# Performance work log

Measured on AMD Instinct MI355X. Metric: run time of the kernel, lower is better.

## Reference

```python
import jax, jax.numpy as jnp
import numpy as np

N_READ = 200000
N_INTRON = 50000
N_EDGES = 2000000
DIMS = [(10, 64), (64, 128), (128, 128), (128, 128), (128, 128), (128, 128)]


def setup_inputs() -> dict:
    key = jax.random.key(0)
    ks = jax.random.split(key, 4 + 2 * len(DIMS) + 3)
    inp = {}
    inp['h_read'] = jax.random.normal(ks[0], (N_READ, 10), dtype=jnp.float32)
    inp['edge_src'] = jax.random.randint(ks[1], (N_EDGES,), 0, N_READ, dtype=jnp.int32)
    inp['edge_dst'] = jax.random.randint(ks[2], (N_EDGES,), 0, N_INTRON, dtype=jnp.int32)
    for i, (fin, fout) in enumerate(DIMS):
        # Glorot-uniform like DGL GraphConv init
        lim = np.sqrt(6.0 / (fin + fout)).astype(np.float32)
        inp[f'W{i}'] = jax.random.uniform(ks[3 + 2 * i], (fin, fout), jnp.float32, -lim, lim)
        inp[f'b{i}'] = jnp.zeros((fout,), jnp.float32)
    inp['atts'] = jax.random.normal(ks[-3], (6,), dtype=jnp.float32)
    inp['fc_w'] = jax.random.normal(ks[-2], (128, 2), dtype=jnp.float32) * 0.05
    inp['fc_b'] = jnp.zeros((2,), jnp.float32)
    return inp


def _graph_conv(feat_src, W, b, src, dst, n_src, n_dst):
    # DGL GraphConv with norm='both': D_src^{-1/2} then sum-aggregate then D_dst^{-1/2}, then linear.
    ones = jnp.ones((src.shape[0],), feat_src.dtype)
    out_deg = jnp.maximum(jax.ops.segment_sum(ones, src, num_segments=n_src), 1.0)
    in_deg = jnp.maximum(jax.ops.segment_sum(ones, dst, num_segments=n_dst), 1.0)
    h = feat_src * jax.lax.rsqrt(out_deg)[:, None]          # [n_src, d]
    agg = jax.ops.segment_sum(h[src], dst, num_segments=n_dst)  # gather + scatter-add
    agg = agg * jax.lax.rsqrt(in_deg)[:, None]
    return agg @ W + b


def reference(h_read, edge_src, edge_dst, W0, W1, W2, W3, W4, W5,
              b0, b1, b2, b3, b4, b5, atts, fc_w, fc_b):
    Ws = [W0, W1, W2, W3, W4, W5]
    bs = [b0, b1, b2, b3, b4, b5]
    h_r = h_read
    h_i = None
    for i in range(6):
        gate = jax.nn.sigmoid(atts[i])
        if i % 2 == 0:
            # read -> intron
            h_i = _graph_conv(h_r, Ws[i], bs[i], edge_src, edge_dst, N_READ, N_INTRON)
            h_i = jax.nn.relu(h_i * gate)
        else:
            # intron -> read (reversed edges)
            h_r = _graph_conv(h_i, Ws[i], bs[i], edge_dst, edge_src, N_INTRON, N_READ)
            h_r = jax.nn.relu(h_r * gate)
    return h_r @ fc_w + fc_b  # [N_READ, 2]
```

## Files before the change

### kernel.cpp

```cpp
#include <hip/hip_runtime.h>

#define N_READ   200000
#define N_INTRON 50000
#define N_EDGES  2000000

#define NB    256
#define EPB   ((N_EDGES + NB - 1) / NB)
#define NBUK  782
#define SH_I  6
#define SH_R  8
#define NITEMS (NBUK * NB)
#define CSH   13
#define NGRP  (N_READ / 4)

typedef float f4 __attribute__((ext_vector_type(4)));
typedef float f2 __attribute__((ext_vector_type(2)));
typedef unsigned u32x4 __attribute__((ext_vector_type(4)));
typedef unsigned short u16x4 __attribute__((ext_vector_type(4)));

static __device__ __forceinline__ unsigned short f2bf(float x) {
  unsigned u = __builtin_bit_cast(unsigned, x);
  u = (u + 0x7fffu + ((u >> 16) & 1u)) >> 16;
  return (unsigned short)u;
}
static __device__ __forceinline__ float blo(unsigned u) {
  return __builtin_bit_cast(float, u << 16);
}
static __device__ __forceinline__ float bhi(unsigned u) {
  return __builtin_bit_cast(float, u & 0xffff0000u);
}

__global__ void kb_hist(const int* __restrict__ src, const int* __restrict__ dst,
                        int* __restrict__ histI, int* __restrict__ histR) {
  __shared__ int hI[1024], hR[1024];
  const int t = threadIdx.x, b = blockIdx.x;
  for (int k = t; k < 1024; k += 256) { hI[k] = 0; hR[k] = 0; }
  __syncthreads();
  const int s0 = b * EPB;
  const int s1 = (s0 + EPB < N_EDGES) ? s0 + EPB : N_EDGES;
  for (int i = s0 + t; i < s1; i += 256) {
    atomicAdd(&hI[dst[i] >> SH_I], 1);
    atomicAdd(&hR[src[i] >> SH_R], 1);
  }
  __syncthreads();
  for (int k = t; k < NBUK; k += 256) {
    histI[k * NB + b] = hI[k];
    histR[k * NB + b] = hR[k];
  }
}

__global__ void k_scan1(const int* __restrict__ cnt, int* __restrict__ rp,
                        int* __restrict__ bsum, int n) {
  __shared__ int lds[256];
  int t = threadIdx.x;
  int i = blockIdx.x * 256 + t;
  int v = (i < n) ? cnt[i] : 0;
  lds[t] = v;
  __syncthreads();
  for (int off = 1; off < 256; off <<= 1) {
    int x = (t >= off) ? lds[t - off] : 0;
    __syncthreads();
    lds[t] += x;
    __syncthreads();
  }
  if (i < n) rp[i + 1] = lds[t];
  if (t == 255) bsum[blockIdx.x] = lds[255];
}

__global__ void k_scan2(int* __restrict__ bsum, int nb) {
  __shared__ int lds[1024];
  int t = threadIdx.x;
  int v = (t < nb) ? bsum[t] : 0;
  lds[t] = v;
  __syncthreads();
  for (int off = 1; off < 1024; off <<= 1) {
    int x = (t >= off) ? lds[t - off] : 0;
    __syncthreads();
    lds[t] += x;
    __syncthreads();
  }
  if (t < nb) bsum[t] = lds[t];
}

__global__ void k_scan3b(int* __restrict__ rp, const int* __restrict__ bsum, int n) {
  int i = blockIdx.x * 256 + threadIdx.x;
  if (i >= n) return;
  int off = (blockIdx.x == 0) ? 0 : bsum[blockIdx.x - 1];
  rp[i + 1] += off;
  if (i == 0) rp[0] = 0;
}

__global__ void kb_scatter(const int* __restrict__ src, const int* __restrict__ dst,
                           const int* __restrict__ scanI, const int* __restrict__ scanR,
                           unsigned* __restrict__ bI, unsigned* __restrict__ bR) {
  __shared__ int cI[1024], cR[1024];
  const int t = threadIdx.x, b = blockIdx.x;
  for (int k = t; k < NBUK; k += 256) {
    cI[k] = scanI[k * NB + b];
    cR[k] = scanR[k * NB + b];
  }
  __syncthreads();
  const int s0 = b * EPB;
  const int s1 = (s0 + EPB < N_EDGES) ? s0 + EPB : N_EDGES;
  for (int i = s0 + t; i < s1; i += 256) {
    int s = src[i], d = dst[i];
    int slot = atomicAdd(&cI[d >> SH_I], 1);
    bI[slot] = ((unsigned)s << SH_I) | (unsigned)(d & 63);
    int slot2 = atomicAdd(&cR[s >> SH_R], 1);
    bR[slot2] = ((unsigned)d << SH_R) | (unsigned)(s & 255);
  }
}

template <int NBINS, int SH, typename PT>
__global__ void kb_fine(const unsigned* __restrict__ bk, const int* __restrict__ scan,
                        int* __restrict__ rp, float* __restrict__ rs,
                        PT* __restrict__ csr, int n_nodes) {
  __shared__ int hist[NBINS], cur[NBINS], lds[256];
  const int t = threadIdx.x, k = blockIdx.x;
  for (int j = t; j < NBINS; j += 256) hist[j] = 0;
  __syncthreads();
  const int s0 = scan[k * NB];
  const int e0 = (k + 1 < NBUK) ? scan[(k + 1) * NB] : N_EDGES;
  for (int i = s0 + t; i < e0; i += 256) atomicAdd(&hist[bk[i] & (NBINS - 1)], 1);
  __syncthreads();
  int v = (t < NBINS) ? hist[t] : 0;
  lds[t] = v;
  __syncthreads();
  for (int off = 1; off < 256; off <<= 1) {
    int x = (t >= off) ? lds[t - off] : 0;
    __syncthreads();
    lds[t] += x;
    __syncthreads();
  }
  if (t < NBINS) {
    int base = s0 + lds[t] - hist[t];
    cur[t] = base;
    int n = k * NBINS + t;
    if (n < n_nodes) {
      rp[n] = base;
      rs[n] = rsqrtf((float)(hist[t] > 0 ? hist[t] : 1));
    }
  }
  if (k == NBUK - 1 && t == 0) rp[n_nodes] = N_EDGES;
  __syncthreads();
  for (int i = s0 + t; i < e0; i += 256) {
    unsigned v2 = bk[i];
    int slot = atomicAdd(&cur[v2 & (NBINS - 1)], 1);
    csr[slot] = (PT)(v2 >> SH);
  }
}

__global__ void kb_fine_r(const unsigned* __restrict__ bk, const int* __restrict__ scan,
                          int* __restrict__ rpg, float* __restrict__ rs,
                          unsigned* __restrict__ recs, int n_nodes) {
  __shared__ int cnt2[64 * 8], cur2[64 * 8], lds[256], cntn[256];
  const int t = threadIdx.x, k = blockIdx.x;
  for (int j = t; j < 512; j += 256) cnt2[j] = 0;
  cntn[t] = 0;
  __syncthreads();
  const int s0 = scan[k * NB];
  const int e0 = (k + 1 < NBUK) ? scan[(k + 1) * NB] : N_EDGES;
  for (int i = s0 + t; i < e0; i += 256) {
    unsigned v = bk[i];
    int rl = v & 255;
    int c = (int)(v >> 8) >> CSH;
    atomicAdd(&cnt2[(rl >> 2) * 8 + c], 1);
    atomicAdd(&cntn[rl], 1);
  }
  __syncthreads();
  int tg = 0;
  if (t < 64) {
#pragma unroll
    for (int c = 0; c < 8; ++c) tg += cnt2[t * 8 + c];
  }
  lds[t] = tg;
  __syncthreads();
  for (int off = 1; off < 64; off <<= 1) {
    int x = (t >= off) ? lds[t - off] : 0;
    __syncthreads();
    lds[t] += x;
    __syncthreads();
  }
  if (t < 64) {
    int base = s0 + lds[t] - tg;
    int run = base;
#pragma unroll
    for (int c = 0; c < 8; ++c) { cur2[t * 8 + c] = run; run += cnt2[t * 8 + c]; }
    int g = k * 64 + t;
    if (g < NGRP) rpg[g] = base;
  }
  {
    int n = k * 256 + t;
    if (n < n_nodes) {
      int d = cntn[t];
      rs[n] = rsqrtf((float)(d > 0 ? d : 1));
    }
  }
  if (k == NBUK - 1 && t == 0) rpg[NGRP] = N_EDGES;
  __syncthreads();
  for (int i = s0 + t; i < e0; i += 256) {
    unsigned v = bk[i];
    int rl = v & 255;
    unsigned intron = v >> 8;
    int c = (int)intron >> CSH;
    int slot = atomicAdd(&cur2[(rl >> 2) * 8 + c], 1);
    recs[slot] = ((unsigned)(rl & 3) << 16) | intron;
  }
}

__global__ void k_prep_h0(const float* __restrict__ h_read, const float* __restrict__ rs_r,
                          float* __restrict__ h16) {
  int i = blockIdx.x * blockDim.x + threadIdx.x;
  if (i >= N_READ * 16) return;
  int n = i >> 4, c = i & 15;
  h16[i] = (c < 10) ? h_read[n * 10 + c] * rs_r[n] : 0.0f;
}

__global__ void k_prep_W0(const float* __restrict__ W0, float* __restrict__ W0p) {
  int i = blockIdx.x * blockDim.x + threadIdx.x;
  if (i >= 16 * 64) return;
  int k = i >> 6, j = i & 63;
  W0p[i] = (k < 10) ? W0[k * 64 + j] : 0.0f;
}

template <int DIN>
__launch_bounds__(256)
__global__ void kx_transform(const unsigned* __restrict__ h32,
                             const float* __restrict__ W,
                             unsigned short* __restrict__ g,
                             int n_src) {
  constexpr int RS = DIN + 4;
  constexpr int HC = DIN / 2;
  __shared__ float rows[32 * RS];
  const int tid = threadIdx.x;
  const int nbase = blockIdx.x * 32;
  for (int idx = tid; idx < 32 * HC; idx += 256) {
    int r = idx / HC, cp = idx % HC;
    int n = nbase + r;
    unsigned u = (n < n_src) ? h32[(size_t)n * HC + cp] : 0u;
    rows[r * RS + cp * 2] = blo(u);
    rows[r * RS + cp * 2 + 1] = bhi(u);
  }
  __syncthreads();
  const int jg = tid % 32, ng = tid / 32;
  const int j0 = jg * 4;
  f4 acc[4];
#pragma unroll
  for (int p = 0; p < 4; ++p) acc[p] = (f4){0.f, 0.f, 0.f, 0.f};
#pragma unroll 2
  for (int k = 0; k < DIN; k += 4) {
    f4 w[4];
#pragma unroll
    for (int u = 0; u < 4; ++u) w[u] = *(const f4*)&W[(k + u) * 128 + j0];
#pragma unroll
    for (int p = 0; p < 4; ++p) {
      f4 r = *(const f4*)&rows[(ng + p * 8) * RS + k];
#pragma unroll
      for (int u = 0; u < 4; ++u) acc[p] += r[u] * w[u];
    }
  }
#pragma unroll
  for (int p = 0; p < 4; ++p) {
    const int n = nbase + ng + p * 8;
    if (n < n_src) {
      u16x4 o = {f2bf(acc[p][0]), f2bf(acc[p][1]), f2bf(acc[p][2]), f2bf(acc[p][3])};
      *(u16x4*)&g[(size_t)n * 128 + j0] = o;
    }
  }
}

template <bool FC>
__launch_bounds__(256)
__global__ void k_sweep2(const unsigned* __restrict__ g32,
                         const int* __restrict__ rpg,
                         const unsigned* __restrict__ recs,
                         const float* __restrict__ rs_dst,
                         const float* __restrict__ bias,
                         const float* __restrict__ atts, int li,
                         unsigned* __restrict__ hout32,
                         const float* __restrict__ fcw, const float* __restrict__ fcb,
                         float* __restrict__ fcout) {
  const int tid = threadIdx.x;
  const int wave = tid >> 6, lane = tid & 63;
  const int slot = lane >> 4, lc = lane & 15;
  const int group = blockIdx.x * 4 + wave;
  const int s = rpg[group], e = rpg[group + 1];

  f4 aA[4], aB[4];
#pragma unroll
  for (int n = 0; n < 4; ++n) {
    aA[n] = (f4){0.f, 0.f, 0.f, 0.f};
    aB[n] = (f4){0.f, 0.f, 0.f, 0.f};
  }

  for (int base = s; base < e; base += 64) {
    int idx = base + lane;
    if (idx > N_EDGES - 1) idx = N_EDGES - 1;
    unsigned rec = recs[idx];
    int m = e - base;
    if (m > 64) m = 64;
    for (int r = 0; r < m; r += 4) {
      unsigned rc = (unsigned)__shfl((int)rec, r + slot, 64);
      int id = (int)(rc & 0xffffu);
      int nl = (int)((rc >> 16) & 3u);
      float act = ((r + slot) < m) ? 1.f : 0.f;
      u32x4 v = *(const u32x4*)(g32 + (size_t)id * 64 + lc * 4);
      f4 vA = {blo(v.x), bhi(v.x), blo(v.y), bhi(v.y)};
      f4 vB = {blo(v.z), bhi(v.z), blo(v.w), bhi(v.w)};
      float m0 = (nl == 0) ? act : 0.f;
      float m1 = (nl == 1) ? act : 0.f;
      float m2 = (nl == 2) ? act : 0.f;
      float m3 = (nl == 3) ? act : 0.f;
      aA[0] += vA * m0; aB[0] += vB * m0;
      aA[1] += vA * m1; aB[1] += vB * m1;
      aA[2] += vA * m2; aB[2] += vB * m2;
      aA[3] += vA * m3; aB[3] += vB * m3;
    }
  }

#pragma unroll
  for (int n = 0; n < 4; ++n) {
#pragma unroll
    for (int j = 0; j < 4; ++j) {
      aA[n][j] += __shfl_xor(aA[n][j], 16);
      aA[n][j] += __shfl_xor(aA[n][j], 32);
      aB[n][j] += __shfl_xor(aB[n][j], 16);
      aB[n][j] += __shfl_xor(aB[n][j], 32);
    }
  }

  f4 sA = aA[0], sB = aB[0];
  if (slot == 1) { sA = aA[1]; sB = aB[1]; }
  if (slot == 2) { sA = aA[2]; sB = aB[2]; }
  if (slot == 3) { sA = aA[3]; sB = aB[3]; }
  const int n = group * 4 + slot;
  const float rsd = rs_dst[n];
  const float gate = 1.f / (1.f + __expf(-atts[li]));
  f4 bA = *(const f4*)&bias[lc * 8];
  f4 bB = *(const f4*)&bias[lc * 8 + 4];
  f4 vA = (sA * rsd + bA) * gate;
  f4 vB = (sB * rsd + bB) * gate;
#pragma unroll
  for (int j = 0; j < 4; ++j) {
    vA[j] = fmaxf(vA[j], 0.f);
    vB[j] = fmaxf(vB[j], 0.f);
  }
  if constexpr (!FC) {
    vA *= rsd;
    vB *= rsd;
    u32x4 o;
    o.x = (unsigned)f2bf(vA[0]) | ((unsigned)f2bf(vA[1]) << 16);
    o.y = (unsigned)f2bf(vA[2]) | ((unsigned)f2bf(vA[3]) << 16);
    o.z = (unsigned)f2bf(vB[0]) | ((unsigned)f2bf(vB[1]) << 16);
    o.w = (unsigned)f2bf(vB[2]) | ((unsigned)f2bf(vB[3]) << 16);
    *(u32x4*)(hout32 + (size_t)n * 64 + lc * 4) = o;
  } else {
    f4 w0 = *(const f4*)&fcw[lc * 16];
    f4 w1 = *(const f4*)&fcw[lc * 16 + 4];
    f4 w2 = *(const f4*)&fcw[lc * 16 + 8];
    f4 w3 = *(const f4*)&fcw[lc * 16 + 12];
    float s0 = vA[0] * w0[0] + vA[1] * w0[2] + vA[2] * w1[0] + vA[3] * w1[2]
             + vB[0] * w2[0] + vB[1] * w2[2] + vB[2] * w3[0] + vB[3] * w3[2];
    float s1 = vA[0] * w0[1] + vA[1] * w0[3] + vA[2] * w1[1] + vA[3] * w1[3]
             + vB[0] * w2[1] + vB[1] * w2[3] + vB[2] * w3[1] + vB[3] * w3[3];
    s0 += __shfl_xor(s0, 1); s0 += __shfl_xor(s0, 2);
    s0 += __shfl_xor(s0, 4); s0 += __shfl_xor(s0, 8);
    s1 += __shfl_xor(s1, 1); s1 += __shfl_xor(s1, 2);
    s1 += __shfl_xor(s1, 4); s1 += __shfl_xor(s1, 8);
    if (lc == 0) {
      fcout[n * 2] = s0 + fcb[0];
      fcout[n * 2 + 1] = s1 + fcb[1];
    }
  }
}

template <int DIN, int DOUT, bool BF16SRC, typename ET>
__launch_bounds__(256)
__global__ void k_layer(const void* __restrict__ hsrc_, const int* __restrict__ rp,
                        const ET* __restrict__ eidx, const float* __restrict__ rs_dst,
                        const float* __restrict__ W, const float* __restrict__ bias,
                        const float* __restrict__ atts, int li,
                        const float* __restrict__ rs_next,
                        void* __restrict__ hout_, int n_dst) {
  constexpr int NT = 32;
  constexpr int RSTR = DIN + 4;
  __shared__ float rows[NT * RSTR];
  __shared__ int rpl[NT + 1];
  const int tid = threadIdx.x;
  const int nbase = blockIdx.x * NT;
  const int team = tid >> 6, lane = tid & 63;
  const float* hs_f = (const float*)hsrc_;
  const unsigned short* hs_b = (const unsigned short*)hsrc_;

  constexpr int LPS = (DIN * (BF16SRC ? 2 : 4)) / 16;
  constexpr int SLOTS = 64 / LPS;
  const int slot = lane / LPS, lc = lane % LPS;

  if (tid <= NT) {
    int nn = nbase + tid;
    if (nn > n_dst) nn = n_dst;
    rpl[tid] = rp[nn];
  }
  __syncthreads();

  {
    int p0 = rpl[team * 8] + lane;
    if (p0 > N_EDGES - 1) p0 = N_EDGES - 1;
    int idsC = (int)eidx[p0];

    for (int t8 = 0; t8 < 8; ++t8) {
      const int t = team * 8 + t8;
      const int e0 = rpl[t], e1 = rpl[t + 1];
      const int deg = e1 - e0;
      int pn = e1 + lane;
      if (pn > N_EDGES - 1) pn = N_EDGES - 1;
      int idsN = (int)eidx[pn];

      f4 accA = {0.f, 0.f, 0.f, 0.f};
      f4 accB = {0.f, 0.f, 0.f, 0.f};
      int processed = 0;
      while (processed < deg) {
        int m = deg - processed;
        if (m > 64) m = 64;
        if (processed > 0) {
          int pr = e0 + processed + lane;
          if (pr > N_EDGES - 1) pr = N_EDGES - 1;
          idsC = (int)eidx[pr];
        }
        for (int r = 0; r < m; r += SLOTS) {
          int idv = __shfl(idsC, r + slot, 64);
          if constexpr (BF16SRC) {
            u32x4 v = *(const u32x4*)(hs_b + (size_t)idv * DIN + lc * 8);
            if (r + slot < m) {
              accA[0] += blo(v.x); accA[1] += bhi(v.x);
              accA[2] += blo(v.y); accA[3] += bhi(v.y);
              accB[0] += blo(v.z); accB[1] += bhi(v.z);
              accB[2] += blo(v.w); accB[3] += bhi(v.w);
            }
          } else {
            f4 v = *(const f4*)(hs_f + (size_t)idv * DIN + lc * 4);
            if (r + slot < m) accA += v;
          }
        }
        processed += m;
      }
      idsC = idsN;

#pragma unroll
      for (int off = LPS; off < 64; off <<= 1) {
#pragma unroll
        for (int k = 0; k < 4; ++k) accA[k] += __shfl_xor(accA[k], off);
        if constexpr (BF16SRC) {
#pragma unroll
          for (int k = 0; k < 4; ++k) accB[k] += __shfl_xor(accB[k], off);
        }
      }
      if (slot == 0) {
        const int n = nbase + t;
        const float rsd = (n < n_dst) ? rs_dst[n] : 0.f;
        if constexpr (BF16SRC) {
          *(f4*)&rows[t * RSTR + lc * 8] = accA * rsd;
          *(f4*)&rows[t * RSTR + lc * 8 + 4] = accB * rsd;
        } else {
          *(f4*)&rows[t * RSTR + lc * 4] = accA * rsd;
        }
      }
    }
  }
  __syncthreads();

  constexpr int JG = DOUT / 4;
  constexpr int NG = 256 / JG;
  constexpr int NPT = NT / NG;
  const int jg = tid % JG, ng = tid / JG;
  const int j0 = jg * 4;

  f4 acc[NPT];
#pragma unroll
  for (int p = 0; p < NPT; ++p) acc[p] = (f4){0.f, 0.f, 0.f, 0.f};

#pragma unroll 2
  for (int k = 0; k < DIN; k += 4) {
    f4 w[4];
#pragma unroll
    for (int u = 0; u < 4; ++u) w[u] = *(const f4*)&W[(k + u) * DOUT + j0];
#pragma unroll
    for (int p = 0; p < NPT; ++p) {
      f4 r = *(const f4*)&rows[(ng + p * NG) * RSTR + k];
#pragma unroll
      for (int u = 0; u < 4; ++u) acc[p] += r[u] * w[u];
    }
  }

  const float gate = 1.f / (1.f + __expf(-atts[li]));
  const f4 b4 = *(const f4*)&bias[j0];
#pragma unroll
  for (int p = 0; p < NPT; ++p) {
    const int nl = ng + p * NG;
    const int n = nbase + nl;
    if (n < n_dst) {
      f4 v = (acc[p] + b4) * gate;
#pragma unroll
      for (int c = 0; c < 4; ++c) v[c] = fmaxf(v[c], 0.f);
      if (rs_next) v *= rs_next[n];
      u16x4 o = {f2bf(v[0]), f2bf(v[1]), f2bf(v[2]), f2bf(v[3])};
      *(u16x4*)&((unsigned short*)hout_)[(size_t)n * DOUT + j0] = o;
    }
  }
}

extern "C" void kernel_launch(void* const* d_in, const int* in_sizes, int n_in,
                              void* d_out, int out_size, void* d_ws, size_t ws_size,
                              hipStream_t stream) {
  const float* h_read = (const float*)d_in[0];
  const int* esrc = (const int*)d_in[1];
  const int* edst = (const int*)d_in[2];
  const float* W0 = (const float*)d_in[3];
  const float* b0 = (const float*)d_in[4];
  const float* W1 = (const float*)d_in[5];
  const float* b1 = (const float*)d_in[6];
  const float* W2 = (const float*)d_in[7];
  const float* b2 = (const float*)d_in[8];
  const float* W3 = (const float*)d_in[9];
  const float* b3 = (const float*)d_in[10];
  const float* W4 = (const float*)d_in[11];
  const float* b4 = (const float*)d_in[12];
  const float* W5 = (const float*)d_in[13];
  const float* b5 = (const float*)d_in[14];
  const float* atts = (const float*)d_in[15];
  const float* fcw = (const float*)d_in[16];
  const float* fcb = (const float*)d_in[17];
  float* out = (float*)d_out;

  char* w = (char*)d_ws;
  size_t off = 0;
  auto alloc = [&](size_t bytes) -> void* {
    void* p = w + off;
    off += (bytes + 15) & ~(size_t)15;
    return p;
  };
  int* rp_i = (int*)alloc((N_INTRON + 1) * 4);
  int* rpg = (int*)alloc((NGRP + 1) * 4);
  int* bsum = (int*)alloc(1024 * 4);
  float* rs_r = (float*)alloc(N_READ * 4);
  float* rs_i = (float*)alloc(N_INTRON * 4);
  unsigned* recs = (unsigned*)alloc((size_t)N_EDGES * 4);
  int* csr_si_i = (int*)alloc(N_EDGES * 4);
  float* W0p = (float*)alloc(16 * 64 * 4);
  int* histI = (int*)alloc(NITEMS * 4);
  int* scanI = (int*)alloc((NITEMS + 1) * 4);
  int* histR = (int*)alloc(NITEMS * 4);
  int* scanR = (int*)alloc((NITEMS + 1) * 4);
  unsigned short* hR = (unsigned short*)alloc((size_t)N_READ * 128 * 2);
  unsigned short* hI = (unsigned short*)alloc((size_t)N_INTRON * 128 * 2);
  unsigned short* g = (unsigned short*)alloc((size_t)N_INTRON * 128 * 2);
  float* h16 = (float*)hR;
  unsigned* bI = (unsigned*)((char*)hR + (size_t)16 * 1024 * 1024);
  unsigned* bR = bI + N_EDGES;

  kb_hist<<<NB, 256, 0, stream>>>(esrc, edst, histI, histR);
  k_scan1<<<NITEMS / 256, 256, 0, stream>>>(histI, scanI, bsum, NITEMS);
  k_scan2<<<1, 1024, 0, stream>>>(bsum, NITEMS / 256);
  k_scan3b<<<NITEMS / 256, 256, 0, stream>>>(scanI, bsum, NITEMS);
  k_scan1<<<NITEMS / 256, 256, 0, stream>>>(histR, scanR, bsum, NITEMS);
  k_scan2<<<1, 1024, 0, stream>>>(bsum, NITEMS / 256);
  k_scan3b<<<NITEMS / 256, 256, 0, stream>>>(scanR, bsum, NITEMS);
  kb_scatter<<<NB, 256, 0, stream>>>(esrc, edst, scanI, scanR, bI, bR);
  kb_fine<64, SH_I, int><<<NBUK, 256, 0, stream>>>(bI, scanI, rp_i, rs_i, csr_si_i, N_INTRON);
  kb_fine_r<<<NBUK, 256, 0, stream>>>(bR, scanR, rpg, rs_r, recs, N_READ);

  k_prep_h0<<<(N_READ * 16 + 255) / 256, 256, 0, stream>>>(h_read, rs_r, h16);
  k_prep_W0<<<4, 256, 0, stream>>>(W0, W0p);

  const int gI = (N_INTRON + 31) / 32;
  const int gT = (N_INTRON + 31) / 32;
  const int gS = NGRP / 4;

  k_layer<16, 64, false, int><<<gI, 256, 0, stream>>>(
      h16, rp_i, csr_si_i, rs_i, W0p, b0, atts, 0, rs_i, hI, N_INTRON);
  kx_transform<64><<<gT, 256, 0, stream>>>((const unsigned*)hI, W1, g, N_INTRON);
  k_sweep2<false><<<gS, 256, 0, stream>>>((const unsigned*)g, rpg, recs, rs_r, b1, atts, 1,
                                          (unsigned*)hR, nullptr, nullptr, nullptr);
  k_layer<128, 128, true, int><<<gI, 256, 0, stream>>>(
      hR, rp_i, csr_si_i, rs_i, W2, b2, atts, 2, rs_i, hI, N_INTRON);
  kx_transform<128><<<gT, 256, 0, stream>>>((const unsigned*)hI, W3, g, N_INTRON);
  k_sweep2<false><<<gS, 256, 0, stream>>>((const unsigned*)g, rpg, recs, rs_r, b3, atts, 3,
                                          (unsigned*)hR, nullptr, nullptr, nullptr);
  k_layer<128, 128, true, int><<<gI, 256, 0, stream>>>(
      hR, rp_i, csr_si_i, rs_i, W4, b4, atts, 4, rs_i, hI, N_INTRON);
  kx_transform<128><<<gT, 256, 0, stream>>>((const unsigned*)hI, W5, g, N_INTRON);
  k_sweep2<true><<<gS, 256, 0, stream>>>((const unsigned*)g, rpg, recs, rs_r, b5, atts, 5,
                                         nullptr, fcw, fcb, out);
}
```

Before: 743.6 us.

## Fuse next-layer weight transform into intron layer kernel and refine read-edge chunks

The separate kx_transform kernel is removed. Each intron-layer block now applies the next layer's weight matrix to its own activated outputs, which it stages in shared memory, and writes the transformed bf16 features straight to g. This drops the hI round trip through global memory and three kernel launches, at the cost of more shared memory and a longer, more register-heavy kernel that also keeps the activation in fp32 instead of rounding it to bf16. The read-side CSR is also sorted into finer intron chunks (32 instead of 8 per group), which should give the sweep gathers better locality but adds more LDS counters in the setup kernel.

```diff
diff --git a/kernel.cpp b/kernel.cpp
--- a/kernel.cpp
+++ b/kernel.cpp
@@ -10,7 +10,8 @@
 #define SH_I  6
 #define SH_R  8
 #define NITEMS (NBUK * NB)
-#define CSH   13
+#define CSH   11
+#define NCHP  32
 #define NGRP  (N_READ / 4)
 
 typedef float f4 __attribute__((ext_vector_type(4)));
@@ -153,9 +154,9 @@
 __global__ void kb_fine_r(const unsigned* __restrict__ bk, const int* __restrict__ scan,
                           int* __restrict__ rpg, float* __restrict__ rs,
                           unsigned* __restrict__ recs, int n_nodes) {
-  __shared__ int cnt2[64 * 8], cur2[64 * 8], lds[256], cntn[256];
+  __shared__ int cnt2[64 * NCHP], cur2[64 * NCHP], lds[256], cntn[256];
   const int t = threadIdx.x, k = blockIdx.x;
-  for (int j = t; j < 512; j += 256) cnt2[j] = 0;
+  for (int j = t; j < 64 * NCHP; j += 256) cnt2[j] = 0;
   cntn[t] = 0;
   __syncthreads();
   const int s0 = scan[k * NB];
@@ -164,14 +165,14 @@
     unsigned v = bk[i];
     int rl = v & 255;
     int c = (int)(v >> 8) >> CSH;
-    atomicAdd(&cnt2[(rl >> 2) * 8 + c], 1);
+    atomicAdd(&cnt2[(rl >> 2) * NCHP + c], 1);
     atomicAdd(&cntn[rl], 1);
   }
   __syncthreads();
   int tg = 0;
   if (t < 64) {
 #pragma unroll
-    for (int c = 0; c < 8; ++c) tg += cnt2[t * 8 + c];
+    for (int c = 0; c < NCHP; ++c) tg += cnt2[t * NCHP + c];
   }
   lds[t] = tg;
   __syncthreads();
@@ -185,7 +186,7 @@
     int base = s0 + lds[t] - tg;
     int run = base;
 #pragma unroll
-    for (int c = 0; c < 8; ++c) { cur2[t * 8 + c] = run; run += cnt2[t * 8 + c]; }
+    for (int c = 0; c < NCHP; ++c) { cur2[t * NCHP + c] = run; run += cnt2[t * NCHP + c]; }
     int g = k * 64 + t;
     if (g < NGRP) rpg[g] = base;
   }
@@ -203,7 +204,7 @@
     int rl = v & 255;
     unsigned intron = v >> 8;
     int c = (int)intron >> CSH;
-    int slot = atomicAdd(&cur2[(rl >> 2) * 8 + c], 1);
+    int slot = atomicAdd(&cur2[(rl >> 2) * NCHP + c], 1);
     recs[slot] = ((unsigned)(rl & 3) << 16) | intron;
   }
 }
@@ -221,52 +222,6 @@
   if (i >= 16 * 64) return;
   int k = i >> 6, j = i & 63;
   W0p[i] = (k < 10) ? W0[k * 64 + j] : 0.0f;
-}
-
-template <int DIN>
-__launch_bounds__(256)
-__global__ void kx_transform(const unsigned* __restrict__ h32,
-                             const float* __restrict__ W,
-                             unsigned short* __restrict__ g,
-                             int n_src) {
-  constexpr int RS = DIN + 4;
-  constexpr int HC = DIN / 2;
-  __shared__ float rows[32 * RS];
-  const int tid = threadIdx.x;
-  const int nbase = blockIdx.x * 32;
-  for (int idx = tid; idx < 32 * HC; idx += 256) {
-    int r = idx / HC, cp = idx % HC;
-    int n = nbase + r;
-    unsigned u = (n < n_src) ? h32[(size_t)n * HC + cp] : 0u;
-    rows[r * RS + cp * 2] = blo(u);
-    rows[r * RS + cp * 2 + 1] = bhi(u);
-  }
-  __syncthreads();
-  const int jg = tid % 32, ng = tid / 32;
-  const int j0 = jg * 4;
-  f4 acc[4];
-#pragma unroll
-  for (int p = 0; p < 4; ++p) acc[p] = (f4){0.f, 0.f, 0.f, 0.f};
-#pragma unroll 2
-  for (int k = 0; k < DIN; k += 4) {
-    f4 w[4];
-#pragma unroll
-    for (int u = 0; u < 4; ++u) w[u] = *(const f4*)&W[(k + u) * 128 + j0];
-#pragma unroll
-    for (int p = 0; p < 4; ++p) {
-      f4 r = *(const f4*)&rows[(ng + p * 8) * RS + k];
-#pragma unroll
-      for (int u = 0; u < 4; ++u) acc[p] += r[u] * w[u];
-    }
-  }
-#pragma unroll
-  for (int p = 0; p < 4; ++p) {
-    const int n = nbase + ng + p * 8;
-    if (n < n_src) {
-      u16x4 o = {f2bf(acc[p][0]), f2bf(acc[p][1]), f2bf(acc[p][2]), f2bf(acc[p][3])};
-      *(u16x4*)&g[(size_t)n * 128 + j0] = o;
-    }
-  }
 }
 
 template <bool FC>
@@ -381,10 +336,14 @@
                         const float* __restrict__ W, const float* __restrict__ bias,
                         const float* __restrict__ atts, int li,
                         const float* __restrict__ rs_next,
-                        void* __restrict__ hout_, int n_dst) {
+                        const float* __restrict__ Wt,
+                        unsigned short* __restrict__ gout,
+                        int n_dst) {
   constexpr int NT = 32;
   constexpr int RSTR = DIN + 4;
-  __shared__ float rows[NT * RSTR];
+  constexpr int RSTR2 = DOUT + 4;
+  constexpr int RMAX = (RSTR > RSTR2) ? RSTR : RSTR2;
+  __shared__ float rows[NT * RMAX];
   __shared__ int rpl[NT + 1];
   const int tid = threadIdx.x;
   const int nbase = blockIdx.x * NT;
@@ -494,17 +453,48 @@
 
   const float gate = 1.f / (1.f + __expf(-atts[li]));
   const f4 b4 = *(const f4*)&bias[j0];
+  f4 vv[NPT];
 #pragma unroll
   for (int p = 0; p < NPT; ++p) {
     const int nl = ng + p * NG;
     const int n = nbase + nl;
+    f4 v = (acc[p] + b4) * gate;
+#pragma unroll
+    for (int c = 0; c < 4; ++c) v[c] = fmaxf(v[c], 0.f);
+    v *= (n < n_dst) ? rs_next[n] : 0.f;
+    vv[p] = v;
+  }
+  __syncthreads();
+#pragma unroll
+  for (int p = 0; p < NPT; ++p) {
+    const int nl = ng + p * NG;
+    *(f4*)&rows[nl * RSTR2 + j0] = vv[p];
+  }
+  __syncthreads();
+
+  const int jg2 = tid % 32, ng2 = tid / 32;
+  const int j02 = jg2 * 4;
+  f4 acc2[4];
+#pragma unroll
+  for (int p = 0; p < 4; ++p) acc2[p] = (f4){0.f, 0.f, 0.f, 0.f};
+#pragma unroll 2
+  for (int k = 0; k < DOUT; k += 4) {
+    f4 w[4];
+#pragma unroll
+    for (int u = 0; u < 4; ++u) w[u] = *(const f4*)&Wt[(k + u) * 128 + j02];
+#pragma unroll
+    for (int p = 0; p < 4; ++p) {
+      f4 r = *(const f4*)&rows[(ng2 + p * 8) * RSTR2 + k];
+#pragma unroll
+      for (int u = 0; u < 4; ++u) acc2[p] += r[u] * w[u];
+    }
+  }
+#pragma unroll
+  for (int p = 0; p < 4; ++p) {
+    const int n = nbase + ng2 + p * 8;
     if (n < n_dst) {
-      f4 v = (acc[p] + b4) * gate;
-#pragma unroll
-      for (int c = 0; c < 4; ++c) v[c] = fmaxf(v[c], 0.f);
-      if (rs_next) v *= rs_next[n];
-      u16x4 o = {f2bf(v[0]), f2bf(v[1]), f2bf(v[2]), f2bf(v[3])};
-      *(u16x4*)&((unsigned short*)hout_)[(size_t)n * DOUT + j0] = o;
+      u16x4 o = {f2bf(acc2[p][0]), f2bf(acc2[p][1]), f2bf(acc2[p][2]), f2bf(acc2[p][3])};
+      *(u16x4*)&gout[(size_t)n * 128 + j02] = o;
     }
   }
 }
@@ -552,7 +542,6 @@
   int* histR = (int*)alloc(NITEMS * 4);
   int* scanR = (int*)alloc((NITEMS + 1) * 4);
   unsigned short* hR = (unsigned short*)alloc((size_t)N_READ * 128 * 2);
-  unsigned short* hI = (unsigned short*)alloc((size_t)N_INTRON * 128 * 2);
   unsigned short* g = (unsigned short*)alloc((size_t)N_INTRON * 128 * 2);
   float* h16 = (float*)hR;
   unsigned* bI = (unsigned*)((char*)hR + (size_t)16 * 1024 * 1024);
@@ -573,22 +562,18 @@
   k_prep_W0<<<4, 256, 0, stream>>>(W0, W0p);
 
   const int gI = (N_INTRON + 31) / 32;
-  const int gT = (N_INTRON + 31) / 32;
   const int gS = NGRP / 4;
 
   k_layer<16, 64, false, int><<<gI, 256, 0, stream>>>(
-      h16, rp_i, csr_si_i, rs_i, W0p, b0, atts, 0, rs_i, hI, N_INTRON);
-  kx_transform<64><<<gT, 256, 0, stream>>>((const unsigned*)hI, W1, g, N_INTRON);
+      h16, rp_i, csr_si_i, rs_i, W0p, b0, atts, 0, rs_i, W1, g, N_INTRON);
   k_sweep2<false><<<gS, 256, 0, stream>>>((const unsigned*)g, rpg, recs, rs_r, b1, atts, 1,
                                           (unsigned*)hR, nullptr, nullptr, nullptr);
   k_layer<128, 128, true, int><<<gI, 256, 0, stream>>>(
-      hR, rp_i, csr_si_i, rs_i, W2, b2, atts, 2, rs_i, hI, N_INTRON);
-  kx_transform<128><<<gT, 256, 0, stream>>>((const unsigned*)hI, W3, g, N_INTRON);
+      hR, rp_i, csr_si_i, rs_i, W2, b2, atts, 2, rs_i, W3, g, N_INTRON);
   k_sweep2<false><<<gS, 256, 0, stream>>>((const unsigned*)g, rpg, recs, rs_r, b3, atts, 3,
                                           (unsigned*)hR, nullptr, nullptr, nullptr);
   k_layer<128, 128, true, int><<<gI, 256, 0, stream>>>(
-      hR, rp_i, csr_si_i, rs_i, W4, b4, atts, 4, rs_i, hI, N_INTRON);
-  kx_transform<128><<<gT, 256, 0, stream>>>((const unsigned*)hI, W5, g, N_INTRON);
+      hR, rp_i, csr_si_i, rs_i, W4, b4, atts, 4, rs_i, W5, g, N_INTRON);
   k_sweep2<true><<<gS, 256, 0, stream>>>((const unsigned*)g, rpg, recs, rs_r, b5, atts, 5,
                                          nullptr, fcw, fcb, out);
 }
```

New measurement: 766.8 us. +3.1%, slower.
